# Optimization experiments

Hardware: AMD Instinct MI355X
Metric: run time of the kernel (lower is better)

Reference implementation:

```python
import jax, jax.numpy as jnp
import numpy as np

COMMITMENT_COST = 0.25


def setup_inputs() -> dict:
    key = jax.random.key(0)
    k1, k2 = jax.random.split(key)
    x = jax.random.normal(k1, (32, 256, 32, 32), dtype=jnp.float32)
    codebook = jax.random.normal(k2, (1024, 256), dtype=jnp.float32) * 0.02
    return {"x": x, "codebook": codebook}


def reference(x, codebook):
    # x: [B, C, H, W] -> z: [B, H, W, C] (NHWC), C = embedding_dim
    B, C, H, W = x.shape
    z = jnp.transpose(x, (0, 2, 3, 1))
    zf = z.reshape(-1, C)  # [N, C], N = B*H*W
    # squared euclidean distance: ||z||^2 - 2 z.e + ||e||^2  -> [N, K]
    d = (
        jnp.sum(zf * zf, axis=-1, keepdims=True)
        - 2.0 * (zf @ codebook.T)
        + jnp.sum(codebook * codebook, axis=-1)
    )
    encoding_indices = jnp.argmin(d, axis=1)  # [N]
    quantized = codebook[encoding_indices].reshape(z.shape)  # [B, H, W, C]

    # training losses (entropy_loss_ratio == 0 -> entropy branch skipped)
    sg = jax.lax.stop_gradient
    e_latent_loss = jnp.mean((sg(quantized) - z) ** 2) * COMMITMENT_COST
    q_latent_loss = jnp.mean((quantized - sg(z)) ** 2)
    quantizer_loss = e_latent_loss + q_latent_loss

    # straight-through estimator
    quantized_st = z + sg(quantized - z)
    out = jnp.transpose(quantized_st, (0, 3, 1, 2))  # back to NCHW
    return out, quantizer_loss, e_latent_loss, q_latent_loss, encoding_indices
```

## Files before the change

kernel.cpp:

```cpp
#include <hip/hip_runtime.h>
#include <cfloat>

#define C_DIM   256
#define HW      1024
#define N_ROWS  32768
#define K_CODES 1024
#define ROWS    64
#define NSUPER  16
#define SUPER_BYTES 32768
#define LISTCAP 128
#define DELTA   0.008f
#define CMASK   0xFFFFFFE0u
#define ZSTRIDE 260

#define OUT_ELEMS 8388608
#define LOSS_OFF  8388608
#define IDX_OFF   8388611

typedef _Float16 half8 __attribute__((ext_vector_type(8)));
typedef _Float16 f16x4 __attribute__((ext_vector_type(4)));
typedef float    f32x4 __attribute__((ext_vector_type(4)));

#define AS1 __attribute__((address_space(1)))
#define AS3 __attribute__((address_space(3)))

#define OFF_EBUF  0
#define OFF_EN    66560
#define OFF_S32   70656
#define OFF_M1W   70912
#define OFF_THR   71424
#define OFF_RES   71680
#define OFF_FIDX  72192
#define OFF_LCNT  72448
#define OFF_LMETA 72704
#define SMEM_BYTES 74752

#define QT_STRIDE 258

#define DPP_MIN(x, ctrl) fminf((x), __int_as_float(__builtin_amdgcn_update_dpp(0, __float_as_int(x), (ctrl), 0xf, 0xf, true)))

__global__ void prep_kernel(const float* __restrict__ cb, float* __restrict__ enorm,
                            char* __restrict__ cb16) {
    int k = blockIdx.x * 4 + (threadIdx.x >> 6);
    int lane = threadIdx.x & 63;
    int c0 = lane * 4;
    float4 v = *(const float4*)(cb + k * C_DIM + c0);
    double s = (double)v.x * v.x + (double)v.y * v.y + (double)v.z * v.z + (double)v.w * v.w;
    #pragma unroll
    for (int m = 1; m < 64; m <<= 1) s += __shfl_xor(s, m, 64);
    if (lane == 0) enorm[k] = (float)s;
    f16x4 h;
    h[0] = (_Float16)v.x; h[1] = (_Float16)v.y; h[2] = (_Float16)v.z; h[3] = (_Float16)v.w;
    int dst = ((k >> 4) << 13) + ((c0 >> 5) << 10) + (((c0 >> 3) & 3) << 8)
            + ((k & 15) << 4) + ((c0 & 7) << 1);
    *(f16x4*)(cb16 + dst) = h;
}

__global__ __launch_bounds__(256, 2) void vq_main(
    const float* __restrict__ x, const float* __restrict__ cb,
    const float* __restrict__ enorm_g, const char* __restrict__ cb16,
    float* __restrict__ out, float* __restrict__ idx_out, float* __restrict__ t2_out)
{
    extern __shared__ char smem[];
    float* zt      = (float*)(smem + OFF_EBUF);
    float* qt      = (float*)(smem + OFF_EBUF);
    char*  ebuf    = smem + OFF_EBUF;
    float* en_lds  = (float*)(smem + OFF_EN);
    float* S32     = (float*)(smem + OFF_S32);
    float* m1w     = (float*)(smem + OFF_M1W);
    float* thr     = (float*)(smem + OFF_THR);
    unsigned long long* res = (unsigned long long*)(smem + OFF_RES);
    int*   fidx    = (int*)(smem + OFF_FIDX);
    int*   lcnt    = (int*)(smem + OFF_LCNT);
    unsigned int* lmeta = (unsigned int*)(smem + OFF_LMETA);

    const int t    = threadIdx.x;
    const int lane = t & 63;
    const int wv   = t >> 6;
    const int wr   = wv >> 1;
    const int wc   = wv & 1;
    const int l15  = lane & 15;
    const int l4   = lane >> 4;
    const int row0 = blockIdx.x * ROWS;
    const int b    = row0 >> 10;
    const int hw0  = row0 & 1023;
    const float* xb = x + b * (C_DIM * HW) + hw0;

    const int qofs = wv * 8192;

    {
        int g   = t & 15;
        int cb4 = t >> 4;
        for (int cc = cb4 * 4; cc < C_DIM; cc += 64) {
            float4 v0 = *(const float4*)(xb + (cc + 0) * HW + g * 4);
            float4 v1 = *(const float4*)(xb + (cc + 1) * HW + g * 4);
            float4 v2 = *(const float4*)(xb + (cc + 2) * HW + g * 4);
            float4 v3 = *(const float4*)(xb + (cc + 3) * HW + g * 4);
            *(float4*)&zt[(g * 4 + 0) * ZSTRIDE + cc] = make_float4(v0.x, v1.x, v2.x, v3.x);
            *(float4*)&zt[(g * 4 + 1) * ZSTRIDE + cc] = make_float4(v0.y, v1.y, v2.y, v3.y);
            *(float4*)&zt[(g * 4 + 2) * ZSTRIDE + cc] = make_float4(v0.z, v1.z, v2.z, v3.z);
            *(float4*)&zt[(g * 4 + 3) * ZSTRIDE + cc] = make_float4(v0.w, v1.w, v2.w, v3.w);
        }
        *(float4*)&en_lds[t * 4] = *(const float4*)(enorm_g + t * 4);
        if (t < 4) lcnt[t] = 0;
    }
    __syncthreads();

    {
        int r = t >> 2, seg = t & 3;
        const float* zr = &zt[r * ZSTRIDE + seg * 64];
        double s = 0.0;
        for (int c = 0; c < 64; c += 4) {
            float4 v = *(const float4*)(zr + c);
            s = fma((double)v.x, (double)v.x, s);
            s = fma((double)v.y, (double)v.y, s);
            s = fma((double)v.z, (double)v.z, s);
            s = fma((double)v.w, (double)v.w, s);
        }
        s += __shfl_xor(s, 1, 64);
        s += __shfl_xor(s, 2, 64);
        if (seg == 0) S32[r] = (float)s;
    }

    half8 af[2][8];
    #pragma unroll
    for (int rt = 0; rt < 2; rt++) {
        int row = wr * 32 + rt * 16 + l15;
        #pragma unroll
        for (int kk = 0; kk < 8; kk++) {
            int c0 = kk * 32 + l4 * 8;
            float4 a  = *(const float4*)&zt[row * ZSTRIDE + c0];
            float4 a2 = *(const float4*)&zt[row * ZSTRIDE + c0 + 4];
            half8 h;
            h[0] = (_Float16)(-2.0f * a.x);  h[1] = (_Float16)(-2.0f * a.y);
            h[2] = (_Float16)(-2.0f * a.z);  h[3] = (_Float16)(-2.0f * a.w);
            h[4] = (_Float16)(-2.0f * a2.x); h[5] = (_Float16)(-2.0f * a2.y);
            h[6] = (_Float16)(-2.0f * a2.z); h[7] = (_Float16)(-2.0f * a2.w);
            af[rt][kk] = h;
        }
    }
    __syncthreads();

    #pragma unroll
    for (int i = 0; i < 8; i++) {
        __builtin_amdgcn_global_load_lds((const AS1 unsigned int*)(cb16 + qofs + i * 1024 + lane * 16),
                                         (AS3 unsigned int*)(ebuf + qofs + i * 1024), 16, 0, 0);
    }

    const int bbase  = (wc << 13) + (l4 << 8) + (l15 << 4);
    const int enbase = wc * 16 + l15;

    float u1[2][4], u2[2][4];
    #pragma unroll
    for (int rt = 0; rt < 2; rt++)
        #pragma unroll
        for (int r2 = 0; r2 < 4; r2++) { u1[rt][r2] = FLT_MAX; u2[rt][r2] = FLT_MAX; }

    for (int sc = 0; sc < NSUPER; sc++) {
        asm volatile("s_waitcnt vmcnt(0)" ::: "memory");
        __builtin_amdgcn_sched_barrier(0);
        __builtin_amdgcn_s_barrier();
        __builtin_amdgcn_sched_barrier(0);

        const char* ebc = ebuf + (sc & 1) * SUPER_BYTES;

        if (sc + 1 < NSUPER) {
            const char* src = cb16 + (sc + 1) * SUPER_BYTES + qofs;
            char* dst = ebuf + ((sc + 1) & 1) * SUPER_BYTES + qofs;
            #pragma unroll
            for (int i = 0; i < 8; i++) {
                __builtin_amdgcn_global_load_lds((const AS1 unsigned int*)(src + i * 1024 + lane * 16),
                                                 (AS3 unsigned int*)(dst + i * 1024), 16, 0, 0);
            }
        }

        {
            const int ch = 2 * sc;
            half8 bf[8];
            #pragma unroll
            for (int kk = 0; kk < 8; kk++)
                bf[kk] = *(const half8*)(ebc + bbase + (kk << 10));
            const float en = en_lds[enbase + ch * 32];
            f32x4 acc0 = {en, en, en, en};
            f32x4 acc1 = {en, en, en, en};
            #pragma unroll
            for (int kk = 0; kk < 8; kk++) {
                acc0 = __builtin_amdgcn_mfma_f32_16x16x32_f16(af[0][kk], bf[kk], acc0, 0, 0, 0);
                acc1 = __builtin_amdgcn_mfma_f32_16x16x32_f16(af[1][kk], bf[kk], acc1, 0, 0, 0);
            }
            #pragma unroll
            for (int r2 = 0; r2 < 4; r2++) {
                float a0 = __uint_as_float((__float_as_uint(acc0[r2]) & CMASK) | (unsigned)ch);
                u2[0][r2] = __builtin_amdgcn_fmed3f(a0, u1[0][r2], u2[0][r2]);
                u1[0][r2] = fminf(u1[0][r2], a0);
                float a1 = __uint_as_float((__float_as_uint(acc1[r2]) & CMASK) | (unsigned)ch);
                u2[1][r2] = __builtin_amdgcn_fmed3f(a1, u1[1][r2], u2[1][r2]);
                u1[1][r2] = fminf(u1[1][r2], a1);
            }
        }
        {
            const int ch = 2 * sc + 1;
            half8 bf[8];
            #pragma unroll
            for (int kk = 0; kk < 8; kk++)
                bf[kk] = *(const half8*)(ebc + 16384 + bbase + (kk << 10));
            const float en = en_lds[enbase + ch * 32];
            f32x4 acc0 = {en, en, en, en};
            f32x4 acc1 = {en, en, en, en};
            #pragma unroll
            for (int kk = 0; kk < 8; kk++) {
                acc0 = __builtin_amdgcn_mfma_f32_16x16x32_f16(af[0][kk], bf[kk], acc0, 0, 0, 0);
                acc1 = __builtin_amdgcn_mfma_f32_16x16x32_f16(af[1][kk], bf[kk], acc1, 0, 0, 0);
            }
            #pragma unroll
            for (int r2 = 0; r2 < 4; r2++) {
                float a0 = __uint_as_float((__float_as_uint(acc0[r2]) & CMASK) | (unsigned)ch);
                u2[0][r2] = __builtin_amdgcn_fmed3f(a0, u1[0][r2], u2[0][r2]);
                u1[0][r2] = fminf(u1[0][r2], a0);
                float a1 = __uint_as_float((__float_as_uint(acc1[r2]) & CMASK) | (unsigned)ch);
                u2[1][r2] = __builtin_amdgcn_fmed3f(a1, u1[1][r2], u2[1][r2]);
                u1[1][r2] = fminf(u1[1][r2], a1);
            }
        }
    }

    #pragma unroll
    for (int rt = 0; rt < 2; rt++) {
        #pragma unroll
        for (int r2 = 0; r2 < 4; r2++) {
            float m = u1[rt][r2];
            m = DPP_MIN(m, 0xB1);
            m = DPP_MIN(m, 0x4E);
            m = DPP_MIN(m, 0x141);
            m = DPP_MIN(m, 0x140);
            if (l15 == 0) m1w[wc * 64 + wr * 32 + rt * 16 + l4 * 4 + r2] = m;
        }
    }
    __syncthreads();
    if (t < 64) {
        thr[t] = fminf(m1w[t], m1w[64 + t]) + DELTA;
        res[t] = ~0ull;
    }
    __syncthreads();

    #pragma unroll
    for (int rt = 0; rt < 2; rt++) {
        #pragma unroll
        for (int r2 = 0; r2 < 4; r2++) {
            int row_l = wr * 32 + rt * 16 + l4 * 4 + r2;
            float tr = thr[row_l];
            if (u1[rt][r2] < tr) {
                int ch1 = (int)(__float_as_uint(u1[rt][r2]) & 31u);
                int code = ch1 * 32 + wc * 16 + l15;
                int slot = atomicAdd(&lcnt[wv], 1);
                if (slot < LISTCAP)
                    lmeta[wv * LISTCAP + slot] = ((unsigned)row_l << 16) | (unsigned)code;
            }
            if (u2[rt][r2] < tr) {
                int ch2 = (int)(__float_as_uint(u2[rt][r2]) & 31u);
                int code = ch2 * 32 + wc * 16 + l15;
                int slot = atomicAdd(&lcnt[wv], 1);
                if (slot < LISTCAP)
                    lmeta[wv * LISTCAP + slot] = ((unsigned)row_l << 16) | (unsigned)code;
            }
        }
    }
    __syncthreads();

    {
        int n = lcnt[wv]; if (n > LISTCAP) n = LISTCAP;
        for (int base = 0; base < n; base += 4) {
            int it = base + l4;
            if (it < n) {
                unsigned meta = lmeta[wv * LISTCAP + it];
                int row  = (int)(meta >> 16);
                int code = (int)(meta & 1023u);
                const float* xr = xb + row;
                const float* er = cb + code * C_DIM;
                double acc = 0.0;
                #pragma unroll
                for (int s2 = 0; s2 < 16; s2++) {
                    int c = l15 + 16 * s2;
                    acc = fma((double)xr[(size_t)c * HW], (double)er[c], acc);
                }
                acc += __shfl_xor(acc, 1, 64);
                acc += __shfl_xor(acc, 2, 64);
                acc += __shfl_xor(acc, 4, 64);
                acc += __shfl_xor(acc, 8, 64);
                if (l15 == 0) {
                    float Mf = (float)acc;
                    float t2 = __fadd_rn(__fsub_rn(S32[row], __fmul_rn(2.0f, Mf)), en_lds[code]);
                    unsigned long long pk =
                        ((unsigned long long)__float_as_uint(t2) << 32) | (unsigned long long)(unsigned)code;
                    atomicMin(&res[row], pk);
                }
            }
        }
    }
    __syncthreads();

    if (t < 64) {
        unsigned long long v = res[t];
        int code = (int)(v & 1023u);
        fidx[t] = code;
        idx_out[row0 + t] = (float)code;
        t2_out[row0 + t] = __uint_as_float((unsigned)(v >> 32));
    }

    float* ob = out + b * (C_DIM * HW) + hw0;
    #pragma unroll
    for (int half = 0; half < 2; half++) {
        __syncthreads();
        for (int idx = t; idx < 32 * 64; idx += 256) {
            int r  = idx >> 6;
            int c4 = idx & 63;
            const float* er = cb + fidx[half * 32 + r] * C_DIM;
            *(float4*)&qt[r * QT_STRIDE + c4 * 4] = *(const float4*)(er + c4 * 4);
        }
        __syncthreads();
        int rr = t & 31;
        int cg = t >> 5;
        for (int cc = cg; cc < C_DIM; cc += 8) {
            ob[cc * HW + half * 32 + rr] = qt[rr * QT_STRIDE + cc];
        }
    }
}

__global__ void loss_kernel(const float* __restrict__ t2min, float* __restrict__ losses) {
    __shared__ double sh[256];
    int t = threadIdx.x;
    double a = 0.0;
    const int per = N_ROWS / 256;
    for (int i = t * per; i < t * per + per; i++) a += (double)t2min[i];
    sh[t] = a;
    __syncthreads();
    for (int s = 128; s > 0; s >>= 1) {
        if (t < s) sh[t] += sh[t + s];
        __syncthreads();
    }
    if (t == 0) {
        double M = sh[0] / (double)OUT_ELEMS;
        losses[0] = (float)(1.25 * M);
        losses[1] = (float)(0.25 * M);
        losses[2] = (float)(M);
    }
}

extern "C" void kernel_launch(void* const* d_in, const int* in_sizes, int n_in,
                              void* d_out, int out_size, void* d_ws, size_t ws_size,
                              hipStream_t stream) {
    const float* x  = (const float*)d_in[0];
    const float* cb = (const float*)d_in[1];
    float* out     = (float*)d_out;
    float* losses  = out + LOSS_OFF;
    float* idx_out = out + IDX_OFF;

    char*  cb16     = (char*)d_ws;
    float* t2ws     = (float*)((char*)d_ws + 524288);
    float* enorm_ws = (float*)((char*)d_ws + 524288 + 131072);

    hipFuncSetAttribute(reinterpret_cast<const void*>(vq_main),
                        hipFuncAttributeMaxDynamicSharedMemorySize, SMEM_BYTES);

    prep_kernel<<<K_CODES / 4, 256, 0, stream>>>(cb, enorm_ws, cb16);
    vq_main<<<N_ROWS / ROWS, 256, SMEM_BYTES, stream>>>(x, cb, enorm_ws, cb16, out, idx_out, t2ws);
    loss_kernel<<<1, 256, 0, stream>>>(t2ws, losses);
}
```

Measured before the change: 66.00 us.

## Split codebook columns across eight waves per block with 512 threads

The main VQ kernel grows from 4 to 8 waves per block. Each wave now covers 16 codes per 64-code super-chunk and runs all 256 channels in one accumulator, instead of two 32-code chunks. Chunk tags in the packed argmin shrink to 4 bits, and the threshold reduction combines four column-wave minima. Prep, copy and output loops are rescaled to 512 threads. The aim is more waves in flight to hide MFMA and LDS latency, at the cost of more barrier participants and extra LDS for the per-wave lists.

```diff
diff --git a/kernel.cpp b/kernel.cpp
--- a/kernel.cpp
+++ b/kernel.cpp
@@ -10,7 +10,7 @@
 #define SUPER_BYTES 32768
 #define LISTCAP 128
 #define DELTA   0.008f
-#define CMASK   0xFFFFFFE0u
+#define CMASK   0xFFFFFFF0u
 #define ZSTRIDE 260
 
 #define OUT_ELEMS 8388608
@@ -28,12 +28,12 @@
 #define OFF_EN    66560
 #define OFF_S32   70656
 #define OFF_M1W   70912
-#define OFF_THR   71424
-#define OFF_RES   71680
-#define OFF_FIDX  72192
-#define OFF_LCNT  72448
-#define OFF_LMETA 72704
-#define SMEM_BYTES 74752
+#define OFF_THR   71936
+#define OFF_RES   72192
+#define OFF_FIDX  72704
+#define OFF_LCNT  72960
+#define OFF_LMETA 73216
+#define SMEM_BYTES 77312
 
 #define QT_STRIDE 258
 
@@ -56,7 +56,7 @@
     *(f16x4*)(cb16 + dst) = h;
 }
 
-__global__ __launch_bounds__(256, 2) void vq_main(
+__global__ __launch_bounds__(512, 4) void vq_main(
     const float* __restrict__ x, const float* __restrict__ cb,
     const float* __restrict__ enorm_g, const char* __restrict__ cb16,
     float* __restrict__ out, float* __restrict__ idx_out, float* __restrict__ t2_out)
@@ -77,8 +77,8 @@
     const int t    = threadIdx.x;
     const int lane = t & 63;
     const int wv   = t >> 6;
-    const int wr   = wv >> 1;
-    const int wc   = wv & 1;
+    const int wr   = wv >> 2;
+    const int wq   = wv & 3;
     const int l15  = lane & 15;
     const int l4   = lane >> 4;
     const int row0 = blockIdx.x * ROWS;
@@ -86,12 +86,12 @@
     const int hw0  = row0 & 1023;
     const float* xb = x + b * (C_DIM * HW) + hw0;
 
-    const int qofs = wv * 8192;
+    const int qofs = wv * 4096;
 
     {
         int g   = t & 15;
         int cb4 = t >> 4;
-        for (int cc = cb4 * 4; cc < C_DIM; cc += 64) {
+        for (int cc = cb4 * 4; cc < C_DIM; cc += 128) {
             float4 v0 = *(const float4*)(xb + (cc + 0) * HW + g * 4);
             float4 v1 = *(const float4*)(xb + (cc + 1) * HW + g * 4);
             float4 v2 = *(const float4*)(xb + (cc + 2) * HW + g * 4);
@@ -101,12 +101,12 @@
             *(float4*)&zt[(g * 4 + 2) * ZSTRIDE + cc] = make_float4(v0.z, v1.z, v2.z, v3.z);
             *(float4*)&zt[(g * 4 + 3) * ZSTRIDE + cc] = make_float4(v0.w, v1.w, v2.w, v3.w);
         }
-        *(float4*)&en_lds[t * 4] = *(const float4*)(enorm_g + t * 4);
-        if (t < 4) lcnt[t] = 0;
-    }
-    __syncthreads();
-
-    {
+        if (t < 256) *(float4*)&en_lds[t * 4] = *(const float4*)(enorm_g + t * 4);
+        if (t < 8) lcnt[t] = 0;
+    }
+    __syncthreads();
+
+    if (t < 256) {
         int r = t >> 2, seg = t & 3;
         const float* zr = &zt[r * ZSTRIDE + seg * 64];
         double s = 0.0;
@@ -142,13 +142,13 @@
     __syncthreads();
 
     #pragma unroll
-    for (int i = 0; i < 8; i++) {
+    for (int i = 0; i < 4; i++) {
         __builtin_amdgcn_global_load_lds((const AS1 unsigned int*)(cb16 + qofs + i * 1024 + lane * 16),
                                          (AS3 unsigned int*)(ebuf + qofs + i * 1024), 16, 0, 0);
     }
 
-    const int bbase  = (wc << 13) + (l4 << 8) + (l15 << 4);
-    const int enbase = wc * 16 + l15;
+    const int bbase  = (wq << 13) + (l4 << 8) + (l15 << 4);
+    const int enbase = wq * 16 + l15;
 
     float u1[2][4], u2[2][4];
     #pragma unroll
@@ -168,59 +168,46 @@
             const char* src = cb16 + (sc + 1) * SUPER_BYTES + qofs;
             char* dst = ebuf + ((sc + 1) & 1) * SUPER_BYTES + qofs;
             #pragma unroll
-            for (int i = 0; i < 8; i++) {
+            for (int i = 0; i < 4; i++) {
                 __builtin_amdgcn_global_load_lds((const AS1 unsigned int*)(src + i * 1024 + lane * 16),
                                                  (AS3 unsigned int*)(dst + i * 1024), 16, 0, 0);
             }
         }
 
+        const float en = en_lds[enbase + sc * 64];
+        f32x4 acc0 = {en, en, en, en};
+        f32x4 acc1 = {en, en, en, en};
         {
-            const int ch = 2 * sc;
-            half8 bf[8];
-            #pragma unroll
-            for (int kk = 0; kk < 8; kk++)
+            half8 bf[4];
+            #pragma unroll
+            for (int kk = 0; kk < 4; kk++)
                 bf[kk] = *(const half8*)(ebc + bbase + (kk << 10));
-            const float en = en_lds[enbase + ch * 32];
-            f32x4 acc0 = {en, en, en, en};
-            f32x4 acc1 = {en, en, en, en};
-            #pragma unroll
-            for (int kk = 0; kk < 8; kk++) {
+            #pragma unroll
+            for (int kk = 0; kk < 4; kk++) {
                 acc0 = __builtin_amdgcn_mfma_f32_16x16x32_f16(af[0][kk], bf[kk], acc0, 0, 0, 0);
                 acc1 = __builtin_amdgcn_mfma_f32_16x16x32_f16(af[1][kk], bf[kk], acc1, 0, 0, 0);
             }
-            #pragma unroll
-            for (int r2 = 0; r2 < 4; r2++) {
-                float a0 = __uint_as_float((__float_as_uint(acc0[r2]) & CMASK) | (unsigned)ch);
-                u2[0][r2] = __builtin_amdgcn_fmed3f(a0, u1[0][r2], u2[0][r2]);
-                u1[0][r2] = fminf(u1[0][r2], a0);
-                float a1 = __uint_as_float((__float_as_uint(acc1[r2]) & CMASK) | (unsigned)ch);
-                u2[1][r2] = __builtin_amdgcn_fmed3f(a1, u1[1][r2], u2[1][r2]);
-                u1[1][r2] = fminf(u1[1][r2], a1);
-            }
         }
         {
-            const int ch = 2 * sc + 1;
-            half8 bf[8];
-            #pragma unroll
-            for (int kk = 0; kk < 8; kk++)
-                bf[kk] = *(const half8*)(ebc + 16384 + bbase + (kk << 10));
-            const float en = en_lds[enbase + ch * 32];
-            f32x4 acc0 = {en, en, en, en};
-            f32x4 acc1 = {en, en, en, en};
-            #pragma unroll
-            for (int kk = 0; kk < 8; kk++) {
-                acc0 = __builtin_amdgcn_mfma_f32_16x16x32_f16(af[0][kk], bf[kk], acc0, 0, 0, 0);
-                acc1 = __builtin_amdgcn_mfma_f32_16x16x32_f16(af[1][kk], bf[kk], acc1, 0, 0, 0);
-            }
-            #pragma unroll
-            for (int r2 = 0; r2 < 4; r2++) {
-                float a0 = __uint_as_float((__float_as_uint(acc0[r2]) & CMASK) | (unsigned)ch);
-                u2[0][r2] = __builtin_amdgcn_fmed3f(a0, u1[0][r2], u2[0][r2]);
-                u1[0][r2] = fminf(u1[0][r2], a0);
-                float a1 = __uint_as_float((__float_as_uint(acc1[r2]) & CMASK) | (unsigned)ch);
-                u2[1][r2] = __builtin_amdgcn_fmed3f(a1, u1[1][r2], u2[1][r2]);
-                u1[1][r2] = fminf(u1[1][r2], a1);
-            }
+            half8 bf[4];
+            #pragma unroll
+            for (int kk = 0; kk < 4; kk++)
+                bf[kk] = *(const half8*)(ebc + bbase + ((kk + 4) << 10));
+            #pragma unroll
+            for (int kk = 0; kk < 4; kk++) {
+                acc0 = __builtin_amdgcn_mfma_f32_16x16x32_f16(af[0][kk + 4], bf[kk], acc0, 0, 0, 0);
+                acc1 = __builtin_amdgcn_mfma_f32_16x16x32_f16(af[1][kk + 4], bf[kk], acc1, 0, 0, 0);
+            }
+        }
+
+        #pragma unroll
+        for (int r2 = 0; r2 < 4; r2++) {
+            float a0 = __uint_as_float((__float_as_uint(acc0[r2]) & CMASK) | (unsigned)sc);
+            u2[0][r2] = __builtin_amdgcn_fmed3f(a0, u1[0][r2], u2[0][r2]);
+            u1[0][r2] = fminf(u1[0][r2], a0);
+            float a1 = __uint_as_float((__float_as_uint(acc1[r2]) & CMASK) | (unsigned)sc);
+            u2[1][r2] = __builtin_amdgcn_fmed3f(a1, u1[1][r2], u2[1][r2]);
+            u1[1][r2] = fminf(u1[1][r2], a1);
         }
     }
 
@@ -233,12 +220,12 @@
             m = DPP_MIN(m, 0x4E);
             m = DPP_MIN(m, 0x141);
             m = DPP_MIN(m, 0x140);
-            if (l15 == 0) m1w[wc * 64 + wr * 32 + rt * 16 + l4 * 4 + r2] = m;
+            if (l15 == 0) m1w[wq * 64 + wr * 32 + rt * 16 + l4 * 4 + r2] = m;
         }
     }
     __syncthreads();
     if (t < 64) {
-        thr[t] = fminf(m1w[t], m1w[64 + t]) + DELTA;
+        thr[t] = fminf(fminf(m1w[t], m1w[64 + t]), fminf(m1w[128 + t], m1w[192 + t])) + DELTA;
         res[t] = ~0ull;
     }
     __syncthreads();
@@ -250,15 +237,15 @@
             int row_l = wr * 32 + rt * 16 + l4 * 4 + r2;
             float tr = thr[row_l];
             if (u1[rt][r2] < tr) {
-                int ch1 = (int)(__float_as_uint(u1[rt][r2]) & 31u);
-                int code = ch1 * 32 + wc * 16 + l15;
+                int sc1 = (int)(__float_as_uint(u1[rt][r2]) & 15u);
+                int code = sc1 * 64 + wq * 16 + l15;
                 int slot = atomicAdd(&lcnt[wv], 1);
                 if (slot < LISTCAP)
                     lmeta[wv * LISTCAP + slot] = ((unsigned)row_l << 16) | (unsigned)code;
             }
             if (u2[rt][r2] < tr) {
-                int ch2 = (int)(__float_as_uint(u2[rt][r2]) & 31u);
-                int code = ch2 * 32 + wc * 16 + l15;
+                int sc2 = (int)(__float_as_uint(u2[rt][r2]) & 15u);
+                int code = sc2 * 64 + wq * 16 + l15;
                 int slot = atomicAdd(&lcnt[wv], 1);
                 if (slot < LISTCAP)
                     lmeta[wv * LISTCAP + slot] = ((unsigned)row_l << 16) | (unsigned)code;
@@ -311,7 +298,7 @@
     #pragma unroll
     for (int half = 0; half < 2; half++) {
         __syncthreads();
-        for (int idx = t; idx < 32 * 64; idx += 256) {
+        for (int idx = t; idx < 32 * 64; idx += 512) {
             int r  = idx >> 6;
             int c4 = idx & 63;
             const float* er = cb + fidx[half * 32 + r] * C_DIM;
@@ -320,7 +307,7 @@
         __syncthreads();
         int rr = t & 31;
         int cg = t >> 5;
-        for (int cc = cg; cc < C_DIM; cc += 8) {
+        for (int cc = cg; cc < C_DIM; cc += 16) {
             ob[cc * HW + half * 32 + rr] = qt[rr * QT_STRIDE + cc];
         }
     }
@@ -363,6 +350,6 @@
                         hipFuncAttributeMaxDynamicSharedMemorySize, SMEM_BYTES);
 
     prep_kernel<<<K_CODES / 4, 256, 0, stream>>>(cb, enorm_ws, cb16);
-    vq_main<<<N_ROWS / ROWS, 256, SMEM_BYTES, stream>>>(x, cb, enorm_ws, cb16, out, idx_out, t2ws);
+    vq_main<<<N_ROWS / ROWS, 512, SMEM_BYTES, stream>>>(x, cb, enorm_ws, cb16, out, idx_out, t2ws);
     loss_kernel<<<1, 256, 0, stream>>>(t2ws, losses);
 }
```

Result: no change. 65.66 us (-0.5%).
